# Kernel tuning notes

Hardware: AMD Instinct MI355X
Metric: run time of the kernel (lower is better)

The kernel has to match this reference:

```python
import jax, jax.numpy as jnp
from jax import lax
import numpy as np

EPS = 1e-4  # self.epsilon
UPS = 16    # 224 / 14 : adaptive_avg_pool2d upsample == nearest repeat when out % in == 0


def _conv1x1(h, W, b):
    # 1x1 conv as channel matmul: h [B,C,H,W], W [O,C]
    return jnp.einsum('bchw,oc->bohw', h, W) + b[None, :, None, None]


def _forward(x, mascaras, Wf, bf, W1, b1, W2, b2, W3, b3, W4, b4, prototypes, last_W, topk_k):
    x = x[:, 0:3, :, :]
    # stand-in backbone: conv 3->512, k16 s16 VALID, ReLU -> [B,512,14,14]
    f = lax.conv_general_dilated(x, Wf, window_strides=(16, 16), padding='VALID')
    f = jax.nn.relu(f + bf[None, :, None, None])
    # add-on bottleneck: 512->256->256->128->128, final sigmoid -> [B,128,14,14]
    h = jax.nn.relu(_conv1x1(f, W1, b1))
    h = jax.nn.relu(_conv1x1(h, W2, b2))
    h = jax.nn.relu(_conv1x1(h, W3, b3))
    h = jax.nn.sigmoid(_conv1x1(h, W4, b4))
    # _l2_convolution with 1x1 prototypes == torch.cdist between patch vectors and prototypes
    f2 = jnp.sum(h * h, axis=1)                    # [B,H,W]
    p2 = jnp.sum(prototypes * prototypes, axis=1)  # [P]
    inner = jnp.einsum('bchw,pc->bphw', h, prototypes)
    d2 = jnp.maximum(f2[:, None] + p2[None, :, None, None] - 2.0 * inner, 0.0)
    distances = jnp.sqrt(d2)                       # [B,P,H,W] (cdist = euclidean, not squared)
    B, P, H, W = distances.shape
    dflat = distances.reshape(B, P, H * W)
    # min_distances: avg of k smallest distances per prototype
    neg_top, _ = lax.top_k(-dflat, topk_k)
    min_distances = jnp.mean(-neg_top, axis=-1)    # [B,P]
    # log similarity
    act = jnp.log((distances + 1.0) / (distances + EPS))
    top_act, _ = lax.top_k(act.reshape(B, P, H * W), topk_k)
    proto_act = jnp.mean(top_act, axis=-1)         # [B,P]
    logits = proto_act @ last_W.T                  # [B,num_classes]
    # adaptive_avg_pool2d 14->224 with integer ratio == repeat by 16 in H and W
    upsampled_activation = jnp.repeat(jnp.repeat(act, UPS, axis=2), UPS, axis=3)
    return logits, min_distances, upsampled_activation


def setup_inputs() -> dict:
    key = jax.random.key(0)
    ks = jax.random.split(key, 12)
    rn = lambda k, s, sc=0.05: jax.random.normal(k, s, jnp.float32) * sc
    return {
        'x': jax.random.normal(ks[0], (16, 3, 224, 224), jnp.float32),
        'mascaras': jax.random.uniform(ks[1], (16, 1, 224, 224), jnp.float32),
        'Wf': rn(ks[2], (512, 3, 16, 16)),
        'bf': jnp.zeros((512,), jnp.float32),
        'W1': rn(ks[3], (256, 512)), 'b1': jnp.zeros((256,), jnp.float32),
        'W2': rn(ks[4], (256, 256)), 'b2': jnp.zeros((256,), jnp.float32),
        'W3': rn(ks[5], (128, 256)), 'b3': jnp.zeros((128,), jnp.float32),
        'W4': rn(ks[6], (128, 128)), 'b4': jnp.zeros((128,), jnp.float32),
        'prototypes': jax.random.uniform(ks[7], (60, 128), jnp.float32),  # torch.rand init
        'last_W': rn(ks[8], (3, 60)),
        'topk_k': 5,
    }


def reference(x, mascaras, Wf, bf, W1, b1, W2, b2, W3, b3, W4, b4, prototypes, last_W, topk_k):
    return _forward(x, mascaras, Wf, bf, W1, b1, W2, b2, W3, b3, W4, b4, prototypes, last_W, topk_k)
```

## Files before the change

kernel.cpp:

```cpp
#include <hip/hip_runtime.h>
#include <hip/hip_bf16.h>

using short8  = __attribute__((ext_vector_type(8))) short;
using ushort8 = __attribute__((ext_vector_type(8))) unsigned short;
using floatx4 = __attribute__((ext_vector_type(4))) float;

#define EPSV 1e-4f

__device__ __forceinline__ unsigned short bfbits(float f) {
  __hip_bfloat16 h = __float2bfloat16(f);
  return *reinterpret_cast<unsigned short*>(&h);
}

__global__ void prep_kernel(const float4* __restrict__ Wf, const float4* __restrict__ W1,
                            const float4* __restrict__ W2, const float4* __restrict__ W3,
                            const float4* __restrict__ W4, ushort4* __restrict__ wdst,
                            const float* __restrict__ x, __hip_bfloat16* __restrict__ A0) {
  if (blockIdx.x < 624) {
    int t = blockIdx.x * 256 + threadIdx.x;
    const float4* src; int off;
    if (t < 98304)       { src = Wf; off = 0; }
    else if (t < 131072) { src = W1; off = 98304; }
    else if (t < 147456) { src = W2; off = 131072; }
    else if (t < 155648) { src = W3; off = 147456; }
    else                 { src = W4; off = 155648; }
    float4 v = src[t - off];
    ushort4 o;
    o.x = bfbits(v.x); o.y = bfbits(v.y); o.z = bfbits(v.z); o.w = bfbits(v.w);
    wdst[t] = o;
  } else {
    int t = (blockIdx.x - 624) * 256 + threadIdx.x;
    int kh = t & 15;
    int rest = t >> 4;
    int c = rest % 3;
    int row = rest / 3;
    int b = row / 196;
    int ij = row - b * 196;
    int i = ij / 14;
    int j = ij - i * 14;
    const float4* s4 = reinterpret_cast<const float4*>(
        x + ((size_t)(b * 3 + c) * 224 + (size_t)(i * 16 + kh)) * 224 + j * 16);
    __hip_bfloat16* dst = A0 + (size_t)row * 768 + c * 256 + kh * 16;
    float4 v0 = s4[0], v1 = s4[1], v2 = s4[2], v3 = s4[3];
    ushort8 o0, o1;
    o0[0] = bfbits(v0.x); o0[1] = bfbits(v0.y); o0[2] = bfbits(v0.z); o0[3] = bfbits(v0.w);
    o0[4] = bfbits(v1.x); o0[5] = bfbits(v1.y); o0[6] = bfbits(v1.z); o0[7] = bfbits(v1.w);
    o1[0] = bfbits(v2.x); o1[1] = bfbits(v2.y); o1[2] = bfbits(v2.z); o1[3] = bfbits(v2.w);
    o1[4] = bfbits(v3.x); o1[5] = bfbits(v3.y); o1[6] = bfbits(v3.z); o1[7] = bfbits(v3.w);
    ushort8* d8 = reinterpret_cast<ushort8*>(dst);
    d8[0] = o0;
    d8[1] = o1;
  }
}

template <int K>
__global__ void gemm_bt(const __hip_bfloat16* __restrict__ A,
                        const __hip_bfloat16* __restrict__ W,
                        const float* __restrict__ bias,
                        __hip_bfloat16* __restrict__ C,
                        int M, int N) {
  const int m0 = blockIdx.x * 64;
  const int n0 = blockIdx.y * 64;
  const int lane = threadIdx.x;
  const int r = lane & 15;
  const int q = lane >> 4;

  const __hip_bfloat16* Abase = A + (size_t)(m0 + r) * K + q * 8;
  const __hip_bfloat16* Wbase = W + (size_t)(n0 + r) * K + q * 8;

  floatx4 acc[4][4] = {};
#pragma unroll 4
  for (int k = 0; k < K; k += 32) {
    short8 a[4], b[4];
#pragma unroll
    for (int i = 0; i < 4; ++i) {
      a[i] = *reinterpret_cast<const short8*>(Abase + (size_t)i * 16 * K + k);
      b[i] = *reinterpret_cast<const short8*>(Wbase + (size_t)i * 16 * K + k);
    }
#pragma unroll
    for (int mi = 0; mi < 4; ++mi)
#pragma unroll
      for (int ni = 0; ni < 4; ++ni)
        acc[mi][ni] = __builtin_amdgcn_mfma_f32_16x16x32_bf16(a[mi], b[ni], acc[mi][ni], 0, 0, 0);
  }

#pragma unroll
  for (int mi = 0; mi < 4; ++mi) {
#pragma unroll
    for (int ni = 0; ni < 4; ++ni) {
      int col = n0 + ni * 16 + r;
      float bv = bias[col];
#pragma unroll
      for (int rr = 0; rr < 4; ++rr) {
        int row = m0 + mi * 16 + q * 4 + rr;
        float v = fmaxf(acc[mi][ni][rr] + bv, 0.0f);
        C[(size_t)row * N + col] = __float2bfloat16(v);
      }
    }
  }
}

__device__ __forceinline__ short8 frag_from_lds(const float* p) {
  float4 f0 = *reinterpret_cast<const float4*>(p);
  float4 f1 = *reinterpret_cast<const float4*>(p + 4);
  short8 a;
  a[0] = bfbits(f0.x); a[1] = bfbits(f0.y); a[2] = bfbits(f0.z); a[3] = bfbits(f0.w);
  a[4] = bfbits(f1.x); a[5] = bfbits(f1.y); a[6] = bfbits(f1.z); a[7] = bfbits(f1.w);
  return a;
}

template <int N, int K, int ACT>
__device__ __forceinline__ void layer_lds(const float* __restrict__ A, int astride,
                                          const __hip_bfloat16* __restrict__ W,
                                          const float* __restrict__ bias,
                                          float* __restrict__ C, int cstride,
                                          int w, int r, int q) {
  constexpr int NA = N / 64;
  const int n0 = w * (N / 4);
  floatx4 acc[NA] = {};
#pragma unroll
  for (int k0 = 0; k0 < K; k0 += 32) {
    short8 a = frag_from_lds(A + r * astride + k0 + q * 8);
#pragma unroll
    for (int ni = 0; ni < NA; ++ni) {
      short8 b = *reinterpret_cast<const short8*>(W + (size_t)(n0 + ni * 16 + r) * K + k0 + q * 8);
      acc[ni] = __builtin_amdgcn_mfma_f32_16x16x32_bf16(a, b, acc[ni], 0, 0, 0);
    }
  }
#pragma unroll
  for (int ni = 0; ni < NA; ++ni) {
    float bv = bias[n0 + ni * 16 + r];
#pragma unroll
    for (int rr = 0; rr < 4; ++rr) {
      float v = acc[ni][rr] + bv;
      v = (ACT == 0) ? fmaxf(v, 0.0f) : 1.0f / (1.0f + __expf(-v));
      C[(q * 4 + rr) * cstride + n0 + ni * 16 + r] = v;
    }
  }
}

__global__ __launch_bounds__(256) void mlp_dist_kernel(
    const __hip_bfloat16* __restrict__ f,
    const __hip_bfloat16* __restrict__ W1B, const float* __restrict__ b1,
    const __hip_bfloat16* __restrict__ W2B, const float* __restrict__ b2,
    const __hip_bfloat16* __restrict__ W3B, const float* __restrict__ b3,
    const __hip_bfloat16* __restrict__ W4B, const float* __restrict__ b4,
    const float* __restrict__ proto,
    float* __restrict__ dist, float* __restrict__ act) {
  __shared__ float bufA[16 * 260];
  __shared__ float bufB[16 * 260];
  __shared__ float ps[60 * 132];
  const int t = threadIdx.x;
  const int w = t >> 6;
  const int lane = t & 63;
  const int r = lane & 15;
  const int q = lane >> 4;
  const int pos0 = blockIdx.x * 16;

  {
    const float4* p4 = reinterpret_cast<const float4*>(proto);
    for (int i = t; i < 1920; i += 256) {
      int p = i >> 5, kc = i & 31;
      *reinterpret_cast<float4*>(&ps[p * 132 + kc * 4]) = p4[i];
    }
  }

  {
    const __hip_bfloat16* Ab = f + (size_t)(pos0 + r) * 512 + q * 8;
    floatx4 acc[4] = {};
#pragma unroll
    for (int k0 = 0; k0 < 512; k0 += 32) {
      short8 a = *reinterpret_cast<const short8*>(Ab + k0);
#pragma unroll
      for (int ni = 0; ni < 4; ++ni) {
        short8 b = *reinterpret_cast<const short8*>(W1B + (size_t)(w * 64 + ni * 16 + r) * 512 + k0 + q * 8);
        acc[ni] = __builtin_amdgcn_mfma_f32_16x16x32_bf16(a, b, acc[ni], 0, 0, 0);
      }
    }
#pragma unroll
    for (int ni = 0; ni < 4; ++ni) {
      float bv = b1[w * 64 + ni * 16 + r];
#pragma unroll
      for (int rr = 0; rr < 4; ++rr) {
        float v = fmaxf(acc[ni][rr] + bv, 0.0f);
        bufA[(q * 4 + rr) * 260 + w * 64 + ni * 16 + r] = v;
      }
    }
  }
  __syncthreads();
  layer_lds<256, 256, 0>(bufA, 260, W2B, b2, bufB, 260, w, r, q);
  __syncthreads();
  layer_lds<128, 256, 0>(bufB, 260, W3B, b3, bufA, 132, w, r, q);
  __syncthreads();
  layer_lds<128, 128, 1>(bufA, 132, W4B, b4, bufB, 132, w, r, q);
  __syncthreads();

  for (int qq = t; qq < 960; qq += 256) {
    int p = qq >> 4;
    int pos = qq & 15;
    const float4* hv4 = reinterpret_cast<const float4*>(&bufB[pos * 132]);
    const float4* pv4 = reinterpret_cast<const float4*>(&ps[p * 132]);
    float s = 0.0f;
#pragma unroll 8
    for (int k = 0; k < 32; ++k) {
      float4 hv = hv4[k];
      float4 pv = pv4[k];
      float d0 = hv.x - pv.x, d1 = hv.y - pv.y, d2 = hv.z - pv.z, d3 = hv.w - pv.w;
      s = fmaf(d0, d0, s); s = fmaf(d1, d1, s); s = fmaf(d2, d2, s); s = fmaf(d3, d3, s);
    }
    float d = sqrtf(s);
    float a = __logf((d + 1.0f) / (d + EPSV));
    int gpos = pos0 + pos;
    int bimg = gpos / 196;
    int hw = gpos - bimg * 196;
    size_t idx = ((size_t)bimg * 60 + p) * 196 + hw;
    dist[idx] = d;
    act[idx] = a;
  }
}

__global__ void topk_kernel(const float* __restrict__ dist,
                            float* __restrict__ proto_act,
                            float* __restrict__ out_mind) {
  const int wid = threadIdx.x >> 6;
  const int lane = threadIdx.x & 63;
  const int u = blockIdx.x * 4 + wid;
  const float* rowp = dist + (size_t)u * 196;

  float v[4];
#pragma unroll
  for (int i = 0; i < 4; ++i) {
    int idx = lane + 64 * i;
    v[i] = (idx < 196) ? rowp[idx] : 1e30f;
  }

  float sd = 0.0f, sa = 0.0f;
#pragma unroll
  for (int round = 0; round < 5; ++round) {
    float lmin = fminf(fminf(v[0], v[1]), fminf(v[2], v[3]));
    float m = lmin;
#pragma unroll
    for (int off = 32; off >= 1; off >>= 1)
      m = fminf(m, __shfl_xor(m, off));
    unsigned long long msk = __ballot(lmin == m);
    int leader = __ffsll((long long)msk) - 1;
    if (lane == leader) {
      if (v[0] == m)      v[0] = 1e30f;
      else if (v[1] == m) v[1] = 1e30f;
      else if (v[2] == m) v[2] = 1e30f;
      else                v[3] = 1e30f;
    }
    sd += m;
    sa += __logf((m + 1.0f) / (m + EPSV));
  }
  if (lane == 0) {
    out_mind[u] = sd * 0.2f;
    proto_act[u] = sa * 0.2f;
  }
}

__global__ void upsample_kernel(const float* __restrict__ act,
                                float* __restrict__ up,
                                const float* __restrict__ proto_act,
                                const float* __restrict__ lastW,
                                float* __restrict__ out_logits) {
  if (blockIdx.x < 47100) {
    int t = blockIdx.x * 256 + threadIdx.x;
    int col4 = t % 56;
    int rem = t / 56;
    int y = rem % 224;
    int bp = rem / 224;
    float v = act[(size_t)bp * 196 + (y >> 4) * 14 + (col4 >> 2)];
    float4 val;
    val.x = v; val.y = v; val.z = v; val.w = v;
    reinterpret_cast<float4*>(up)[t] = val;
  } else {
    int t = threadIdx.x;
    if (t < 48) {
      int b = t / 3, c = t - b * 3;
      float s = 0.0f;
      for (int p = 0; p < 60; ++p)
        s += proto_act[b * 60 + p] * lastW[c * 60 + p];
      out_logits[t] = s;
    }
  }
}

extern "C" void kernel_launch(void* const* d_in, const int* in_sizes, int n_in,
                              void* d_out, int out_size, void* d_ws, size_t ws_size,
                              hipStream_t stream) {
  const float* x     = (const float*)d_in[0];
  const float* Wf    = (const float*)d_in[2];
  const float* bf    = (const float*)d_in[3];
  const float* W1    = (const float*)d_in[4];
  const float* b1    = (const float*)d_in[5];
  const float* W2    = (const float*)d_in[6];
  const float* b2    = (const float*)d_in[7];
  const float* W3    = (const float*)d_in[8];
  const float* b3    = (const float*)d_in[9];
  const float* W4    = (const float*)d_in[10];
  const float* b4    = (const float*)d_in[11];
  const float* proto = (const float*)d_in[12];
  const float* lastW = (const float*)d_in[13];

  char* ws = (char*)d_ws;
  __hip_bfloat16* WfB = (__hip_bfloat16*)(ws + 0);
  __hip_bfloat16* W1B = (__hip_bfloat16*)(ws + 786432);
  __hip_bfloat16* W2B = (__hip_bfloat16*)(ws + 1048576);
  __hip_bfloat16* W3B = (__hip_bfloat16*)(ws + 1179648);
  __hip_bfloat16* W4B = (__hip_bfloat16*)(ws + 1245184);
  __hip_bfloat16* A0 = (__hip_bfloat16*)(ws + 1310720);
  __hip_bfloat16* f  = (__hip_bfloat16*)(ws + 6128128);
  float* dist = (float*)(ws + 9339392);
  float* act  = (float*)(ws + 10092032);
  float* pact = (float*)(ws + 10844672);

  float* out        = (float*)d_out;
  float* out_logits = out;
  float* out_mind   = out + 48;
  float* out_up     = out + 1008;

  prep_kernel<<<1212, 256, 0, stream>>>((const float4*)Wf, (const float4*)W1,
                                        (const float4*)W2, (const float4*)W3,
                                        (const float4*)W4, (ushort4*)WfB, x, A0);
  gemm_bt<768><<<dim3(49, 8), 64, 0, stream>>>(A0, WfB, bf, f, 3136, 512);
  mlp_dist_kernel<<<196, 256, 0, stream>>>(f, W1B, b1, W2B, b2, W3B, b3, W4B, b4,
                                           proto, dist, act);
  topk_kernel<<<240, 256, 0, stream>>>(dist, pact, out_mind);
  upsample_kernel<<<47101, 256, 0, stream>>>(act, out_up, pact, lastW, out_logits);
}
```

Measured before the change: 279.7 us.

## Fuse backbone patch-conv GEMM into the MLP/distance kernel

Removes the separate gemm_bt launch for the 16x16 stride-16 patch conv and computes it inside mlp_dist_kernel for each 16-position tile, keeping the 512-channel features in shared memory instead of writing and re-reading a bf16 intermediate in global memory. The first add-on layer now reads its input from LDS through layer_lds. This saves a kernel launch and a global round trip. In exchange, each of the 196 blocks now carries the full K=768 by N=512 conv GEMM with only 16 rows, so it reads the whole Wf from L2 once per block. Larger LDS use (about 33KB more) may also reduce occupancy.

```diff
diff --git a/kernel.cpp b/kernel.cpp
--- a/kernel.cpp
+++ b/kernel.cpp
@@ -53,53 +53,6 @@
   }
 }
 
-template <int K>
-__global__ void gemm_bt(const __hip_bfloat16* __restrict__ A,
-                        const __hip_bfloat16* __restrict__ W,
-                        const float* __restrict__ bias,
-                        __hip_bfloat16* __restrict__ C,
-                        int M, int N) {
-  const int m0 = blockIdx.x * 64;
-  const int n0 = blockIdx.y * 64;
-  const int lane = threadIdx.x;
-  const int r = lane & 15;
-  const int q = lane >> 4;
-
-  const __hip_bfloat16* Abase = A + (size_t)(m0 + r) * K + q * 8;
-  const __hip_bfloat16* Wbase = W + (size_t)(n0 + r) * K + q * 8;
-
-  floatx4 acc[4][4] = {};
-#pragma unroll 4
-  for (int k = 0; k < K; k += 32) {
-    short8 a[4], b[4];
-#pragma unroll
-    for (int i = 0; i < 4; ++i) {
-      a[i] = *reinterpret_cast<const short8*>(Abase + (size_t)i * 16 * K + k);
-      b[i] = *reinterpret_cast<const short8*>(Wbase + (size_t)i * 16 * K + k);
-    }
-#pragma unroll
-    for (int mi = 0; mi < 4; ++mi)
-#pragma unroll
-      for (int ni = 0; ni < 4; ++ni)
-        acc[mi][ni] = __builtin_amdgcn_mfma_f32_16x16x32_bf16(a[mi], b[ni], acc[mi][ni], 0, 0, 0);
-  }
-
-#pragma unroll
-  for (int mi = 0; mi < 4; ++mi) {
-#pragma unroll
-    for (int ni = 0; ni < 4; ++ni) {
-      int col = n0 + ni * 16 + r;
-      float bv = bias[col];
-#pragma unroll
-      for (int rr = 0; rr < 4; ++rr) {
-        int row = m0 + mi * 16 + q * 4 + rr;
-        float v = fmaxf(acc[mi][ni][rr] + bv, 0.0f);
-        C[(size_t)row * N + col] = __float2bfloat16(v);
-      }
-    }
-  }
-}
-
 __device__ __forceinline__ short8 frag_from_lds(const float* p) {
   float4 f0 = *reinterpret_cast<const float4*>(p);
   float4 f1 = *reinterpret_cast<const float4*>(p + 4);
@@ -140,13 +93,15 @@
 }
 
 __global__ __launch_bounds__(256) void mlp_dist_kernel(
-    const __hip_bfloat16* __restrict__ f,
+    const __hip_bfloat16* __restrict__ A0,
+    const __hip_bfloat16* __restrict__ WfB, const float* __restrict__ bias0,
     const __hip_bfloat16* __restrict__ W1B, const float* __restrict__ b1,
     const __hip_bfloat16* __restrict__ W2B, const float* __restrict__ b2,
     const __hip_bfloat16* __restrict__ W3B, const float* __restrict__ b3,
     const __hip_bfloat16* __restrict__ W4B, const float* __restrict__ b4,
     const float* __restrict__ proto,
     float* __restrict__ dist, float* __restrict__ act) {
+  __shared__ float bufF[16 * 516];
   __shared__ float bufA[16 * 260];
   __shared__ float bufB[16 * 260];
   __shared__ float ps[60 * 132];
@@ -166,27 +121,28 @@
   }
 
   {
-    const __hip_bfloat16* Ab = f + (size_t)(pos0 + r) * 512 + q * 8;
-    floatx4 acc[4] = {};
-#pragma unroll
-    for (int k0 = 0; k0 < 512; k0 += 32) {
+    const __hip_bfloat16* Ab = A0 + (size_t)(pos0 + r) * 768 + q * 8;
+    floatx4 acc[8] = {};
+#pragma unroll 4
+    for (int k0 = 0; k0 < 768; k0 += 32) {
       short8 a = *reinterpret_cast<const short8*>(Ab + k0);
 #pragma unroll
-      for (int ni = 0; ni < 4; ++ni) {
-        short8 b = *reinterpret_cast<const short8*>(W1B + (size_t)(w * 64 + ni * 16 + r) * 512 + k0 + q * 8);
+      for (int ni = 0; ni < 8; ++ni) {
+        short8 b = *reinterpret_cast<const short8*>(
+            WfB + (size_t)(w * 128 + ni * 16 + r) * 768 + k0 + q * 8);
         acc[ni] = __builtin_amdgcn_mfma_f32_16x16x32_bf16(a, b, acc[ni], 0, 0, 0);
       }
     }
 #pragma unroll
-    for (int ni = 0; ni < 4; ++ni) {
-      float bv = b1[w * 64 + ni * 16 + r];
-#pragma unroll
-      for (int rr = 0; rr < 4; ++rr) {
-        float v = fmaxf(acc[ni][rr] + bv, 0.0f);
-        bufA[(q * 4 + rr) * 260 + w * 64 + ni * 16 + r] = v;
-      }
-    }
-  }
+    for (int ni = 0; ni < 8; ++ni) {
+      float bv = bias0[w * 128 + ni * 16 + r];
+#pragma unroll
+      for (int rr = 0; rr < 4; ++rr)
+        bufF[(q * 4 + rr) * 516 + w * 128 + ni * 16 + r] = fmaxf(acc[ni][rr] + bv, 0.0f);
+    }
+  }
+  __syncthreads();
+  layer_lds<256, 512, 0>(bufF, 516, W1B, b1, bufA, 260, w, r, q);
   __syncthreads();
   layer_lds<256, 256, 0>(bufA, 260, W2B, b2, bufB, 260, w, r, q);
   __syncthreads();
@@ -310,7 +266,6 @@
   __hip_bfloat16* W3B = (__hip_bfloat16*)(ws + 1179648);
   __hip_bfloat16* W4B = (__hip_bfloat16*)(ws + 1245184);
   __hip_bfloat16* A0 = (__hip_bfloat16*)(ws + 1310720);
-  __hip_bfloat16* f  = (__hip_bfloat16*)(ws + 6128128);
   float* dist = (float*)(ws + 9339392);
   float* act  = (float*)(ws + 10092032);
   float* pact = (float*)(ws + 10844672);
@@ -323,9 +278,8 @@
   prep_kernel<<<1212, 256, 0, stream>>>((const float4*)Wf, (const float4*)W1,
                                         (const float4*)W2, (const float4*)W3,
                                         (const float4*)W4, (ushort4*)WfB, x, A0);
-  gemm_bt<768><<<dim3(49, 8), 64, 0, stream>>>(A0, WfB, bf, f, 3136, 512);
-  mlp_dist_kernel<<<196, 256, 0, stream>>>(f, W1B, b1, W2B, b2, W3B, b3, W4B, b4,
-                                           proto, dist, act);
+  mlp_dist_kernel<<<196, 256, 0, stream>>>(A0, WfB, bf, W1B, b1, W2B, b2,
+                                           W3B, b3, W4B, b4, proto, dist, act);
   topk_kernel<<<240, 256, 0, stream>>>(dist, pact, out_mind);
   upsample_kernel<<<47101, 256, 0, stream>>>(act, out_up, pact, lastW, out_logits);
 }
```

New measurement: 274.0 us. 2.0% less time.
